# Kernel optimization log

Measured on AMD Instinct MI355X. Metric: run time of the kernel, lower is better.

## Reference

```python
import jax, jax.numpy as jnp
import numpy as np

N = 65536
D_IN = 784
H = 20
D_OUT = 10
N_MID = 28  # fc2..fc29, all Linear(20,20)


def setup_inputs() -> dict:
    key = jax.random.key(0)
    ks = jax.random.split(key, 8)
    # PyTorch Linear default init: U(-1/sqrt(fan_in), 1/sqrt(fan_in)); uniform is fine for a reference.
    def uni(k, shape, fan_in):
        bound = 1.0 / np.sqrt(fan_in)
        return jax.random.uniform(k, shape, jnp.float32, -bound, bound)
    x = jax.random.normal(ks[0], (N, D_IN), jnp.float32)
    W1 = uni(ks[1], (H, D_IN), D_IN)
    b1 = uni(ks[2], (H,), D_IN)
    Wmid = uni(ks[3], (N_MID, H, H), H)   # stacked fc2..fc29 weights
    bmid = uni(ks[4], (N_MID, H), H)
    W30 = uni(ks[5], (D_OUT, H), H)
    b30 = uni(ks[6], (D_OUT,), H)
    return {"x": x, "W1": W1, "b1": b1, "Wmid": Wmid, "bmid": bmid, "W30": W30, "b30": b30}


def reference(x, W1, b1, Wmid, bmid, W30, b30):
    # fc1 + relu
    h = jax.nn.relu(x @ W1.T + b1)  # [N, 20]
    # fc2..fc29 + relu, identical structure -> scan over stacked params
    def step(h, wb):
        W, b = wb
        return jax.nn.relu(h @ W.T + b), None
    h, _ = jax.lax.scan(step, h, (Wmid, bmid))
    # fc30 (no relu)
    return h @ W30.T + b30  # [N, 10]
```

## Files before the change

kernel.cpp:

```cpp
#include <hip/hip_runtime.h>

typedef __attribute__((ext_vector_type(8))) short short8;
typedef __attribute__((ext_vector_type(16))) float f32x16;
typedef unsigned short ushort16_t;

#define MFMA(A, B, C) __builtin_amdgcn_mfma_f32_32x32x16_bf16(A, B, C, 0, 0, 0)

__device__ __forceinline__ float4 ldf4(const float* p) { return *(const float4*)p; }
__device__ __forceinline__ short8 ld8(const void* p) { return *(const short8*)p; }

__device__ __forceinline__ short8 mk8(unsigned w0, unsigned w1, unsigned w2, unsigned w3) {
    union { unsigned u[4]; short8 s; } t;
    t.u[0] = w0; t.u[1] = w1; t.u[2] = w2; t.u[3] = w3;
    return t.s;
}
__device__ __forceinline__ unsigned packhi2(float a, float b) {
    return __builtin_amdgcn_perm(__float_as_uint(b), __float_as_uint(a), 0x07060302u);
}
__device__ __forceinline__ float lopart(float v) {
    return v - __uint_as_float(__float_as_uint(v) & 0xFFFF0000u);
}
__device__ __forceinline__ void plswap(unsigned& lo, unsigned& hi) {
    asm("v_permlane32_swap_b32 %0, %1" : "+v"(lo), "+v"(hi));
}

__device__ __forceinline__ ushort16_t h16(float x) { return (ushort16_t)(__float_as_uint(x) >> 16); }
__device__ __forceinline__ float fh(ushort16_t u) { return __uint_as_float(((unsigned)u) << 16); }

__global__ void prepack(const float* __restrict__ W1,
                        const float* __restrict__ Wmid, const float* __restrict__ bmid,
                        const float* __restrict__ W30, const float* __restrict__ b30,
                        ushort16_t* __restrict__ w1t, ushort16_t* __restrict__ midt)
{
    const int tid = blockIdx.x * 256 + threadIdx.x;
    const int nth = gridDim.x * 256;
    for (int i = tid; i < 49 * 512; i += nth) {
        const int j = i & 7, hf = (i >> 3) & 1, o = (i >> 4) & 31, s = i >> 9;
        const float v = (o < 20) ? W1[o * 784 + s * 16 + hf * 8 + j] : 0.f;
        w1t[i] = h16(v);
    }
    for (int e = tid; e < 29 * 64; e += nth) {
        const int hf = e & 1, o = (e >> 1) & 31, l = e >> 6;
        ushort16_t v[32];
#pragma unroll
        for (int i = 0; i < 32; ++i) v[i] = 0;
        const bool lastl = (l == 28);
        const int omax = lastl ? 10 : 20;
        if (o < omax) {
            const float* wr = lastl ? (W30 + o * 20) : (Wmid + l * 400 + o * 20);
            const float bias = lastl ? b30[o] : bmid[l * 20 + o];
#pragma unroll
            for (int j = 0; j < 8; ++j) {
                const float w = wr[hf * 8 + j];
                v[j]      = h16(w);
                v[16 + j] = h16(w - fh(h16(w)));
            }
            if (hf == 0) {
#pragma unroll
                for (int j = 0; j < 4; ++j) {
                    const float w = wr[16 + j];
                    v[8 + j]  = h16(w);
                    v[24 + j] = h16(w - fh(h16(w)));
                }
                v[12] = h16(bias);
                v[13] = h16(bias - fh(h16(bias)));
            }
        }
#pragma unroll
        for (int i = 0; i < 32; ++i) midt[e * 32 + i] = v[i];
    }
}

__global__ __launch_bounds__(256, 4)
void mlp_main(const float* __restrict__ x, const float* __restrict__ b1p,
              const ushort16_t* __restrict__ w1t, const ushort16_t* __restrict__ midt,
              float* __restrict__ out, int nrows)
{
    __shared__ float red[2][16][64];

    const int lane = threadIdx.x & 63;
    const int wv   = threadIdx.x >> 6;
    const int kw   = wv & 1;
    const int tl   = wv >> 1;
    const int tile = blockIdx.x * 2 + tl;
    const int r0   = tile * 32;
    if (r0 >= nrows) return;
    const int colr = lane & 31;
    const int half = lane >> 5;
    const int row  = r0 + colr;

    const int sbeg = kw ? 25 : 0;
    const float* xp = x + (size_t)row * 784 + half * 8 + sbeg * 16;
    const ushort16_t* at = w1t + sbeg * 512 + colr * 16 + half * 8;

    f32x16 acc;
#pragma unroll
    for (int r = 0; r < 16; ++r) acc[r] = 0.f;

    float4 a0 = ldf4(xp),      a1 = ldf4(xp + 4);
    float4 a2 = ldf4(xp + 16), a3 = ldf4(xp + 20);
    short8 Aa0 = ld8(at), Aa1 = ld8(at + 512);

#pragma unroll 1
    for (int cc = 0; cc < 6; ++cc) {
        const float* q = xp + (2 * cc + 1) * 32;
        const float4 c0 = ldf4(q),      c1 = ldf4(q + 4);
        const float4 c2 = ldf4(q + 16), c3 = ldf4(q + 20);
        const short8 Ab0 = ld8(at + (2 * cc + 1) * 1024);
        const short8 Ab1 = ld8(at + (2 * cc + 1) * 1024 + 512);
        acc = MFMA(Aa0, mk8(packhi2(a0.x, a0.y), packhi2(a0.z, a0.w),
                            packhi2(a1.x, a1.y), packhi2(a1.z, a1.w)), acc);
        acc = MFMA(Aa1, mk8(packhi2(a2.x, a2.y), packhi2(a2.z, a2.w),
                            packhi2(a3.x, a3.y), packhi2(a3.z, a3.w)), acc);
        if (cc < 5) {
            const float* q2 = xp + (2 * cc + 2) * 32;
            a0 = ldf4(q2);      a1 = ldf4(q2 + 4);
            a2 = ldf4(q2 + 16); a3 = ldf4(q2 + 20);
            Aa0 = ld8(at + (2 * cc + 2) * 1024);
            Aa1 = ld8(at + (2 * cc + 2) * 1024 + 512);
        }
        acc = MFMA(Ab0, mk8(packhi2(c0.x, c0.y), packhi2(c0.z, c0.w),
                            packhi2(c1.x, c1.y), packhi2(c1.z, c1.w)), acc);
        acc = MFMA(Ab1, mk8(packhi2(c2.x, c2.y), packhi2(c2.z, c2.w),
                            packhi2(c3.x, c3.y), packhi2(c3.z, c3.w)), acc);
    }
    if (!kw) {
        const float4 t0 = ldf4(xp + 384), t1 = ldf4(xp + 388);
        const short8 At = ld8(at + 24 * 512);
        acc = MFMA(At, mk8(packhi2(t0.x, t0.y), packhi2(t0.z, t0.w),
                           packhi2(t1.x, t1.y), packhi2(t1.z, t1.w)), acc);
    }

    if (kw) {
#pragma unroll
        for (int r = 0; r < 16; ++r) red[tl][r][lane] = acc[r];
    }
    __syncthreads();
    if (kw) return;
#pragma unroll
    for (int r = 0; r < 16; ++r) acc[r] += red[tl][r][lane];

    float Hv[16];
#pragma unroll
    for (int r = 0; r < 16; ++r) {
        const int o = (r & 3) + 8 * (r >> 2) + 4 * half;
        Hv[r] = fmaxf(acc[r] + b1p[o < 20 ? o : 0], 0.f);
    }

    const char* ap = (const char*)midt + (size_t)(colr * 2 + half) * 64;
#pragma unroll 1
    for (int l = 0; l < 29; ++l) {
        const short8 A0h = ld8(ap), A1h = ld8(ap + 16);
        const short8 A0l = ld8(ap + 32), A1l = ld8(ap + 48);
        ap += 4096;

        unsigned plo0 = packhi2(Hv[0], Hv[1]), plo1 = packhi2(Hv[2], Hv[3]);
        unsigned phi0 = packhi2(Hv[4], Hv[5]), phi1 = packhi2(Hv[6], Hv[7]);
        plswap(plo0, phi0); plswap(plo1, phi1);
        const short8 B0h = mk8(plo0, plo1, phi0, phi1);

        unsigned qlo0 = packhi2(lopart(Hv[0]), lopart(Hv[1]));
        unsigned qlo1 = packhi2(lopart(Hv[2]), lopart(Hv[3]));
        unsigned qhi0 = packhi2(lopart(Hv[4]), lopart(Hv[5]));
        unsigned qhi1 = packhi2(lopart(Hv[6]), lopart(Hv[7]));
        plswap(qlo0, qhi0); plswap(qlo1, qhi1);
        const short8 B0l = mk8(qlo0, qlo1, qhi0, qhi1);

        const short8 B1h = mk8(half ? 0u : packhi2(Hv[8], Hv[9]),
                               half ? 0u : packhi2(Hv[10], Hv[11]),
                               half ? 0u : 0x00003F80u, 0u);
        const short8 B1l = mk8(half ? 0u : packhi2(lopart(Hv[8]), lopart(Hv[9])),
                               half ? 0u : packhi2(lopart(Hv[10]), lopart(Hv[11])),
                               half ? 0u : 0x3F800000u, 0u);

        f32x16 d;
#pragma unroll
        for (int r = 0; r < 16; ++r) d[r] = 0.f;
        d = MFMA(A0h, B0h, d);
        d = MFMA(A0l, B0h, d);
        d = MFMA(A0h, B0l, d);
        d = MFMA(A1h, B1h, d);
        d = MFMA(A1l, B1h, d);
        d = MFMA(A1h, B1l, d);

        if (l < 28) {
#pragma unroll
            for (int r = 0; r < 16; ++r) Hv[r] = fmaxf(d[r], 0.f);
        } else {
#pragma unroll
            for (int r = 0; r < 16; ++r) {
                const int o = (r & 3) + 8 * (r >> 2) + 4 * half;
                if (o < 10) out[(size_t)row * 10 + o] = d[r];
            }
        }
    }
}

extern "C" void kernel_launch(void* const* d_in, const int* in_sizes, int n_in,
                              void* d_out, int out_size, void* d_ws, size_t ws_size,
                              hipStream_t stream)
{
    const float* x    = (const float*)d_in[0];
    const float* W1   = (const float*)d_in[1];
    const float* b1   = (const float*)d_in[2];
    const float* Wmid = (const float*)d_in[3];
    const float* bmid = (const float*)d_in[4];
    const float* W30  = (const float*)d_in[5];
    const float* b30  = (const float*)d_in[6];
    float* out = (float*)d_out;

    ushort16_t* w1t  = (ushort16_t*)d_ws;
    ushort16_t* midt = (ushort16_t*)((char*)d_ws + 50176);

    const int nrows = in_sizes[0] / 784;
    prepack<<<32, 256, 0, stream>>>(W1, Wmid, bmid, W30, b30, w1t, midt);
    const int tiles = (nrows + 31) / 32;
    const int grid  = (tiles + 1) / 2;
    mlp_main<<<grid, 256, 0, stream>>>(x, b1, w1t, midt, out, nrows);
}
```

Measured before the change: 61.77 us.

## Stage x tile into LDS as bf16 with coalesced loads, split K over four waves

Each block now handles one 32-row tile. All 256 threads first load the contiguous x tile with coalesced float4 loads, convert it to bf16 and store it in shared memory. The fc1 K-dimension is then split across four waves reading B from LDS, with a three-way reduction through reused shared memory. The mid-layer weight table is relaid so each lane's 16-byte loads are contiguous across lanes. This targets the uncoalesced per-row strided global reads of the old fc1 loop. In exchange it adds about 50KB of LDS per block, lowers the occupancy hint to 3, and adds extra barriers.

```diff
diff --git a/kernel.cpp b/kernel.cpp
--- a/kernel.cpp
+++ b/kernel.cpp
@@ -2,7 +2,7 @@
 
 typedef __attribute__((ext_vector_type(8))) short short8;
 typedef __attribute__((ext_vector_type(16))) float f32x16;
-typedef unsigned short ushort16_t;
+typedef unsigned short ushort_t;
 
 #define MFMA(A, B, C) __builtin_amdgcn_mfma_f32_32x32x16_bf16(A, B, C, 0, 0, 0)
 
@@ -23,14 +23,13 @@
 __device__ __forceinline__ void plswap(unsigned& lo, unsigned& hi) {
     asm("v_permlane32_swap_b32 %0, %1" : "+v"(lo), "+v"(hi));
 }
-
-__device__ __forceinline__ ushort16_t h16(float x) { return (ushort16_t)(__float_as_uint(x) >> 16); }
-__device__ __forceinline__ float fh(ushort16_t u) { return __uint_as_float(((unsigned)u) << 16); }
+__device__ __forceinline__ ushort_t h16(float x) { return (ushort_t)(__float_as_uint(x) >> 16); }
+__device__ __forceinline__ float fh(ushort_t u) { return __uint_as_float(((unsigned)u) << 16); }
 
 __global__ void prepack(const float* __restrict__ W1,
                         const float* __restrict__ Wmid, const float* __restrict__ bmid,
                         const float* __restrict__ W30, const float* __restrict__ b30,
-                        ushort16_t* __restrict__ w1t, ushort16_t* __restrict__ midt)
+                        ushort_t* __restrict__ w1t, ushort_t* __restrict__ midt)
 {
     const int tid = blockIdx.x * 256 + threadIdx.x;
     const int nth = gridDim.x * 256;
@@ -39,9 +38,10 @@
         const float v = (o < 20) ? W1[o * 784 + s * 16 + hf * 8 + j] : 0.f;
         w1t[i] = h16(v);
     }
-    for (int e = tid; e < 29 * 64; e += nth) {
-        const int hf = e & 1, o = (e >> 1) & 31, l = e >> 6;
-        ushort16_t v[32];
+    for (int e2 = tid; e2 < 29 * 64; e2 += nth) {
+        const int ee = e2 & 63, l = e2 >> 6;
+        const int o = ee & 31, hf = ee >> 5;
+        ushort_t v[32];
 #pragma unroll
         for (int i = 0; i < 32; ++i) v[i] = 0;
         const bool lastl = (l == 28);
@@ -67,92 +67,88 @@
             }
         }
 #pragma unroll
-        for (int i = 0; i < 32; ++i) midt[e * 32 + i] = v[i];
-    }
-}
-
-__global__ __launch_bounds__(256, 4)
-void mlp_main(const float* __restrict__ x, const float* __restrict__ b1p,
-              const ushort16_t* __restrict__ w1t, const ushort16_t* __restrict__ midt,
+        for (int f = 0; f < 4; ++f)
+#pragma unroll
+            for (int j = 0; j < 8; ++j)
+                midt[l * 2048 + f * 512 + ee * 8 + j] = v[f * 8 + j];
+    }
+}
+
+__global__ __launch_bounds__(256, 3)
+void mlp_main(const float* __restrict__ x, const float* __restrict__ b1,
+              const ushort_t* __restrict__ w1t, const ushort_t* __restrict__ midt,
               float* __restrict__ out, int nrows)
 {
-    __shared__ float red[2][16][64];
-
-    const int lane = threadIdx.x & 63;
-    const int wv   = threadIdx.x >> 6;
-    const int kw   = wv & 1;
-    const int tl   = wv >> 1;
-    const int tile = blockIdx.x * 2 + tl;
-    const int r0   = tile * 32;
+    __shared__ ushort_t xt[32 * 792];
+
+    const int tid  = threadIdx.x;
+    const int lane = tid & 63;
+    const int wv   = tid >> 6;
+    const int r0   = blockIdx.x * 32;
     if (r0 >= nrows) return;
     const int colr = lane & 31;
     const int half = lane >> 5;
     const int row  = r0 + colr;
 
-    const int sbeg = kw ? 25 : 0;
-    const float* xp = x + (size_t)row * 784 + half * 8 + sbeg * 16;
-    const ushort16_t* at = w1t + sbeg * 512 + colr * 16 + half * 8;
+    const float4* xg = (const float4*)(x + (size_t)r0 * 784);
+#define STG(IDX, V) do {                                                  \
+        const unsigned _i = (unsigned)(IDX);                              \
+        const unsigned _r = (_i * 10700u) >> 21;          \
+        const unsigned _c = _i - _r * 196u;                               \
+        *(uint2*)&xt[_r * 792 + _c * 4] =                                 \
+            make_uint2(packhi2((V).x, (V).y), packhi2((V).z, (V).w));     \
+    } while (0)
+
+#pragma unroll 1
+    for (int i = 0; i < 24; i += 4) {
+        const float4 v0 = xg[(i + 0) * 256 + tid];
+        const float4 v1 = xg[(i + 1) * 256 + tid];
+        const float4 v2 = xg[(i + 2) * 256 + tid];
+        const float4 v3 = xg[(i + 3) * 256 + tid];
+        STG((i + 0) * 256 + tid, v0);
+        STG((i + 1) * 256 + tid, v1);
+        STG((i + 2) * 256 + tid, v2);
+        STG((i + 3) * 256 + tid, v3);
+    }
+    if (tid < 128) { const float4 v = xg[6144 + tid]; STG(6144 + tid, v); }
+    __syncthreads();
 
     f32x16 acc;
 #pragma unroll
     for (int r = 0; r < 16; ++r) acc[r] = 0.f;
-
-    float4 a0 = ldf4(xp),      a1 = ldf4(xp + 4);
-    float4 a2 = ldf4(xp + 16), a3 = ldf4(xp + 20);
-    short8 Aa0 = ld8(at), Aa1 = ld8(at + 512);
-
 #pragma unroll 1
-    for (int cc = 0; cc < 6; ++cc) {
-        const float* q = xp + (2 * cc + 1) * 32;
-        const float4 c0 = ldf4(q),      c1 = ldf4(q + 4);
-        const float4 c2 = ldf4(q + 16), c3 = ldf4(q + 20);
-        const short8 Ab0 = ld8(at + (2 * cc + 1) * 1024);
-        const short8 Ab1 = ld8(at + (2 * cc + 1) * 1024 + 512);
-        acc = MFMA(Aa0, mk8(packhi2(a0.x, a0.y), packhi2(a0.z, a0.w),
-                            packhi2(a1.x, a1.y), packhi2(a1.z, a1.w)), acc);
-        acc = MFMA(Aa1, mk8(packhi2(a2.x, a2.y), packhi2(a2.z, a2.w),
-                            packhi2(a3.x, a3.y), packhi2(a3.z, a3.w)), acc);
-        if (cc < 5) {
-            const float* q2 = xp + (2 * cc + 2) * 32;
-            a0 = ldf4(q2);      a1 = ldf4(q2 + 4);
-            a2 = ldf4(q2 + 16); a3 = ldf4(q2 + 20);
-            Aa0 = ld8(at + (2 * cc + 2) * 1024);
-            Aa1 = ld8(at + (2 * cc + 2) * 1024 + 512);
-        }
-        acc = MFMA(Ab0, mk8(packhi2(c0.x, c0.y), packhi2(c0.z, c0.w),
-                            packhi2(c1.x, c1.y), packhi2(c1.z, c1.w)), acc);
-        acc = MFMA(Ab1, mk8(packhi2(c2.x, c2.y), packhi2(c2.z, c2.w),
-                            packhi2(c3.x, c3.y), packhi2(c3.z, c3.w)), acc);
-    }
-    if (!kw) {
-        const float4 t0 = ldf4(xp + 384), t1 = ldf4(xp + 388);
-        const short8 At = ld8(at + 24 * 512);
-        acc = MFMA(At, mk8(packhi2(t0.x, t0.y), packhi2(t0.z, t0.w),
-                           packhi2(t1.x, t1.y), packhi2(t1.z, t1.w)), acc);
-    }
-
-    if (kw) {
-#pragma unroll
-        for (int r = 0; r < 16; ++r) red[tl][r][lane] = acc[r];
+    for (int s = wv; s <= 48; s += 4) {
+        const short8 A = ld8(w1t + s * 512 + colr * 16 + half * 8);
+        const short8 B = ld8(&xt[colr * 792 + s * 16 + half * 8]);
+        acc = MFMA(A, B, acc);
     }
     __syncthreads();
-    if (kw) return;
-#pragma unroll
-    for (int r = 0; r < 16; ++r) acc[r] += red[tl][r][lane];
+
+    float* red = (float*)xt;
+    if (wv) {
+#pragma unroll
+        for (int r = 0; r < 16; ++r) red[(wv - 1) * 1024 + r * 64 + lane] = acc[r];
+    }
+    __syncthreads();
+    if (wv) return;
+#pragma unroll
+    for (int r = 0; r < 16; ++r)
+        acc[r] += (red[r * 64 + lane] + red[1024 + r * 64 + lane]) + red[2048 + r * 64 + lane];
 
     float Hv[16];
 #pragma unroll
     for (int r = 0; r < 16; ++r) {
         const int o = (r & 3) + 8 * (r >> 2) + 4 * half;
-        Hv[r] = fmaxf(acc[r] + b1p[o < 20 ? o : 0], 0.f);
-    }
-
-    const char* ap = (const char*)midt + (size_t)(colr * 2 + half) * 64;
+        Hv[r] = fmaxf(acc[r] + b1[o < 20 ? o : 0], 0.f);
+    }
+
+    const ushort_t* ap = midt + lane * 8;
 #pragma unroll 1
     for (int l = 0; l < 29; ++l) {
-        const short8 A0h = ld8(ap), A1h = ld8(ap + 16);
-        const short8 A0l = ld8(ap + 32), A1l = ld8(ap + 48);
-        ap += 4096;
+        const short8 A0h = ld8(ap + l * 2048);
+        const short8 A1h = ld8(ap + l * 2048 + 512);
+        const short8 A0l = ld8(ap + l * 2048 + 1024);
+        const short8 A1l = ld8(ap + l * 2048 + 1536);
 
         unsigned plo0 = packhi2(Hv[0], Hv[1]), plo1 = packhi2(Hv[2], Hv[3]);
         unsigned phi0 = packhi2(Hv[4], Hv[5]), phi1 = packhi2(Hv[6], Hv[7]);
@@ -194,6 +190,7 @@
             }
         }
     }
+#undef STG
 }
 
 extern "C" void kernel_launch(void* const* d_in, const int* in_sizes, int n_in,
@@ -209,12 +206,11 @@
     const float* b30  = (const float*)d_in[6];
     float* out = (float*)d_out;
 
-    ushort16_t* w1t  = (ushort16_t*)d_ws;
-    ushort16_t* midt = (ushort16_t*)((char*)d_ws + 50176);
+    ushort_t* w1t  = (ushort_t*)d_ws;
+    ushort_t* midt = (ushort_t*)((char*)d_ws + 50176);
 
     const int nrows = in_sizes[0] / 784;
     prepack<<<32, 256, 0, stream>>>(W1, Wmid, bmid, W30, b30, w1t, midt);
-    const int tiles = (nrows + 31) / 32;
-    const int grid  = (tiles + 1) / 2;
+    const int grid = (nrows + 31) / 32;
     mlp_main<<<grid, 256, 0, stream>>>(x, b1, w1t, midt, out, nrows);
 }
```

Result: slower. 85.22 us (+38.0%).
